# Kernel tuning notes

Hardware: AMD Instinct MI355X
Metric: run time of the kernel (lower is better)

The kernel has to match this reference:

```python
import jax, jax.numpy as jnp
import numpy as np

B, S, H, F, E, TOPK = 4, 2048, 1024, 3584, 8, 2
W_SCALE = 0.02  # keep router logits / activations numerically sane


def setup_inputs() -> dict:
    key = jax.random.key(0)
    k1, k2, k3, k4, k5 = jax.random.split(key, 5)
    return {
        "hidden_states": jax.random.normal(k1, (B, S, H), dtype=jnp.float32),
        "gate_w": jax.random.normal(k2, (E, H), dtype=jnp.float32) * W_SCALE,
        "w1": jax.random.normal(k3, (E, F, H), dtype=jnp.float32) * W_SCALE,
        "w2": jax.random.normal(k4, (E, H, F), dtype=jnp.float32) * W_SCALE,
        "w3": jax.random.normal(k5, (E, F, H), dtype=jnp.float32) * W_SCALE,
        "top_k": TOPK,
    }


def reference(hidden_states, gate_w, w1, w2, w3, top_k):
    b, s, h = hidden_states.shape
    x = hidden_states.reshape(-1, h)                       # [T, H]
    router_logits = x @ gate_w.T                           # [T, E]
    probs = jax.nn.softmax(router_logits.astype(jnp.float32), axis=-1)
    routing_weights, selected_experts = jax.lax.top_k(probs, top_k)  # [T, k]
    routing_weights = routing_weights / routing_weights.sum(axis=-1, keepdims=True)
    routing_weights = routing_weights.astype(x.dtype)
    n_experts = gate_w.shape[0]
    # combine weights: [T, E], zero for unselected experts
    combine = (jax.nn.one_hot(selected_experts, n_experts, dtype=routing_weights.dtype)
               * routing_weights[..., None]).sum(axis=1)
    out = jnp.zeros_like(x)
    for e in range(n_experts):
        hgate = jax.nn.silu(x @ w1[e].T) * (x @ w3[e].T)   # [T, F]
        out = out + (hgate @ w2[e].T) * combine[:, e:e + 1]
    return out.reshape(b, s, h), router_logits
```

## Files before the change

### kernel.cpp

```cpp
#include <hip/hip_runtime.h>
#include <hip/hip_bf16.h>
#include <stdint.h>

#define T_TOK 8192
#define H_DIM 1024
#define F_DIM 3584
#define E_NUM 8

#define BM 128
#define BN 128
#define BK 32
#define LDT 40

typedef __attribute__((ext_vector_type(8))) short bf16x8;
typedef __attribute__((ext_vector_type(4))) float f32x4;

__device__ __forceinline__ short f2bf(float f) {
    union { float f; uint32_t u; } v; v.f = f;
    uint32_t r = v.u + 0x7fffu + ((v.u >> 16) & 1u);
    return (short)(r >> 16);
}

__device__ __forceinline__ void cvt16_store(const float* __restrict__ src, short* dst) {
    const f32x4* p = (const f32x4*)src;
    f32x4 v0 = p[0], v1 = p[1], v2 = p[2], v3 = p[3];
    bf16x8 s0, s1;
    s0[0]=f2bf(v0[0]); s0[1]=f2bf(v0[1]); s0[2]=f2bf(v0[2]); s0[3]=f2bf(v0[3]);
    s0[4]=f2bf(v1[0]); s0[5]=f2bf(v1[1]); s0[6]=f2bf(v1[2]); s0[7]=f2bf(v1[3]);
    s1[0]=f2bf(v2[0]); s1[1]=f2bf(v2[1]); s1[2]=f2bf(v2[2]); s1[3]=f2bf(v2[3]);
    s1[4]=f2bf(v3[0]); s1[5]=f2bf(v3[1]); s1[6]=f2bf(v3[2]); s1[7]=f2bf(v3[3]);
    *(bf16x8*)dst = s0;
    *((bf16x8*)dst + 1) = s1;
}

__device__ __forceinline__ void zero16_store(short* dst) {
    bf16x8 z;
    #pragma unroll
    for (int i = 0; i < 8; i++) z[i] = 0;
    *(bf16x8*)dst = z;
    *((bf16x8*)dst + 1) = z;
}

__global__ void router_kernel(const float* __restrict__ x,
                              const float* __restrict__ gate_w,
                              float* __restrict__ logits_out,
                              int* __restrict__ counts,
                              int* __restrict__ lists,
                              float* __restrict__ wgt) {
    int wave = (blockIdx.x * blockDim.x + threadIdx.x) >> 6;
    int lane = threadIdx.x & 63;
    if (wave >= T_TOK) return;
    const float* xr = x + (size_t)wave * H_DIM;

    float acc[E_NUM];
    #pragma unroll
    for (int e = 0; e < E_NUM; e++) acc[e] = 0.f;

    for (int i = lane; i < H_DIM; i += 64) {
        float xv = xr[i];
        #pragma unroll
        for (int e = 0; e < E_NUM; e++) acc[e] += xv * gate_w[e * H_DIM + i];
    }
    #pragma unroll
    for (int off = 32; off > 0; off >>= 1) {
        #pragma unroll
        for (int e = 0; e < E_NUM; e++) acc[e] += __shfl_xor(acc[e], off);
    }

    if (lane == 0) {
        int t = wave;
        #pragma unroll
        for (int e = 0; e < E_NUM; e++) logits_out[t * E_NUM + e] = acc[e];
        int i0 = 0; float v0 = acc[0];
        #pragma unroll
        for (int e = 1; e < E_NUM; e++) if (acc[e] > v0) { v0 = acc[e]; i0 = e; }
        int i1 = -1; float v1 = -1e30f;
        #pragma unroll
        for (int e = 0; e < E_NUM; e++) if (e != i0 && acc[e] > v1) { v1 = acc[e]; i1 = e; }
        float e1 = __expf(v1 - v0);
        float inv = 1.f / (1.f + e1);
        int a0 = 2 * t, a1 = 2 * t + 1;
        wgt[a0] = inv;
        wgt[a1] = e1 * inv;
        int p0 = atomicAdd(&counts[i0], 1);
        lists[i0 * T_TOK + p0] = a0;
        int p1 = atomicAdd(&counts[i1], 1);
        lists[i1 * T_TOK + p1] = a1;
    }
}

__global__ __launch_bounds__(256, 2)
void gemm1_kernel(const float* __restrict__ x,
                  const float* __restrict__ w1,
                  const float* __restrict__ w3,
                  const int* __restrict__ counts,
                  const int* __restrict__ lists,
                  unsigned short* __restrict__ hgate) {
    const int e = blockIdx.z;
    const int count = counts[e];
    const int mbase = blockIdx.y * BM;
    if (mbase >= count) return;
    const int nbase = blockIdx.x * BN;

    __shared__ short As[BM * LDT];
    __shared__ short B1s[BN * LDT];
    __shared__ short B3s[BN * LDT];

    const int tid = threadIdx.x;
    const int r = tid >> 1;
    const int half = tid & 1;

    const float* arow = nullptr;
    {
        int m = mbase + r;
        if (m < count) {
            int a = lists[e * T_TOK + m];
            arow = x + (size_t)(a >> 1) * H_DIM;
        }
    }
    const float* b1row = w1 + ((size_t)e * F_DIM + (nbase + r)) * H_DIM;
    const float* b3row = w3 + ((size_t)e * F_DIM + (nbase + r)) * H_DIM;

    const int lane = tid & 63;
    const int wid = tid >> 6;
    const int wm = wid >> 1, wn = wid & 1;
    const int lr = lane & 15, lq = lane >> 4;

    f32x4 acc1[4][4], acc3[4][4];
    #pragma unroll
    for (int i = 0; i < 4; i++)
        #pragma unroll
        for (int j = 0; j < 4; j++) {
            acc1[i][j] = (f32x4){0.f, 0.f, 0.f, 0.f};
            acc3[i][j] = (f32x4){0.f, 0.f, 0.f, 0.f};
        }

    for (int k0 = 0; k0 < H_DIM; k0 += BK) {
        const int koff = k0 + half * 16;
        short* adst = &As[r * LDT + half * 16];
        if (arow) cvt16_store(arow + koff, adst); else zero16_store(adst);
        cvt16_store(b1row + koff, &B1s[r * LDT + half * 16]);
        cvt16_store(b3row + koff, &B3s[r * LDT + half * 16]);
        __syncthreads();

        bf16x8 af[4], b1f[4], b3f[4];
        #pragma unroll
        for (int i = 0; i < 4; i++)
            af[i] = *(const bf16x8*)&As[(wm * 64 + i * 16 + lr) * LDT + lq * 8];
        #pragma unroll
        for (int j = 0; j < 4; j++) {
            b1f[j] = *(const bf16x8*)&B1s[(wn * 64 + j * 16 + lr) * LDT + lq * 8];
            b3f[j] = *(const bf16x8*)&B3s[(wn * 64 + j * 16 + lr) * LDT + lq * 8];
        }
        #pragma unroll
        for (int i = 0; i < 4; i++)
            #pragma unroll
            for (int j = 0; j < 4; j++) {
                acc1[i][j] = __builtin_amdgcn_mfma_f32_16x16x32_bf16(af[i], b1f[j], acc1[i][j], 0, 0, 0);
                acc3[i][j] = __builtin_amdgcn_mfma_f32_16x16x32_bf16(af[i], b3f[j], acc3[i][j], 0, 0, 0);
            }
        __syncthreads();
    }

    #pragma unroll
    for (int i = 0; i < 4; i++) {
        #pragma unroll
        for (int rg = 0; rg < 4; rg++) {
            int mm = mbase + wm * 64 + i * 16 + lq * 4 + rg;
            if (mm >= count) continue;
            int a = lists[e * T_TOK + mm];
            unsigned short* hrow = hgate + (size_t)a * F_DIM + nbase;
            #pragma unroll
            for (int j = 0; j < 4; j++) {
                float g = acc1[i][j][rg];
                float u = acc3[i][j][rg];
                float s = (g / (1.f + __expf(-g))) * u;
                hrow[wn * 64 + j * 16 + lr] = (unsigned short)f2bf(s);
            }
        }
    }
}

__global__ __launch_bounds__(256, 2)
void gemm2_kernel(const unsigned short* __restrict__ hgate,
                  const float* __restrict__ w2,
                  const int* __restrict__ counts,
                  const int* __restrict__ lists,
                  const float* __restrict__ wgt,
                  float* __restrict__ out) {
    const int e = blockIdx.z;
    const int count = counts[e];
    const int mbase = blockIdx.y * BM;
    if (mbase >= count) return;
    const int nbase = blockIdx.x * BN;

    __shared__ short As[BM * LDT];
    __shared__ short Bs[BN * LDT];

    const int tid = threadIdx.x;
    const int r = tid >> 1;
    const int half = tid & 1;

    const unsigned short* arow = nullptr;
    {
        int m = mbase + r;
        if (m < count) {
            int a = lists[e * T_TOK + m];
            arow = hgate + (size_t)a * F_DIM;
        }
    }
    const float* brow = w2 + ((size_t)e * H_DIM + (nbase + r)) * F_DIM;

    const int lane = tid & 63;
    const int wid = tid >> 6;
    const int wm = wid >> 1, wn = wid & 1;
    const int lr = lane & 15, lq = lane >> 4;

    f32x4 acc[4][4];
    #pragma unroll
    for (int i = 0; i < 4; i++)
        #pragma unroll
        for (int j = 0; j < 4; j++) acc[i][j] = (f32x4){0.f, 0.f, 0.f, 0.f};

    for (int k0 = 0; k0 < F_DIM; k0 += BK) {
        const int koff = k0 + half * 16;
        short* adst = &As[r * LDT + half * 16];
        if (arow) {
            const bf16x8* p = (const bf16x8*)(arow + koff);
            *(bf16x8*)adst = p[0];
            *((bf16x8*)adst + 1) = p[1];
        } else {
            zero16_store(adst);
        }
        cvt16_store(brow + koff, &Bs[r * LDT + half * 16]);
        __syncthreads();

        bf16x8 af[4], bf[4];
        #pragma unroll
        for (int i = 0; i < 4; i++)
            af[i] = *(const bf16x8*)&As[(wm * 64 + i * 16 + lr) * LDT + lq * 8];
        #pragma unroll
        for (int j = 0; j < 4; j++)
            bf[j] = *(const bf16x8*)&Bs[(wn * 64 + j * 16 + lr) * LDT + lq * 8];
        #pragma unroll
        for (int i = 0; i < 4; i++)
            #pragma unroll
            for (int j = 0; j < 4; j++)
                acc[i][j] = __builtin_amdgcn_mfma_f32_16x16x32_bf16(af[i], bf[j], acc[i][j], 0, 0, 0);
        __syncthreads();
    }

    #pragma unroll
    for (int i = 0; i < 4; i++) {
        #pragma unroll
        for (int rg = 0; rg < 4; rg++) {
            int mm = mbase + wm * 64 + i * 16 + lq * 4 + rg;
            if (mm >= count) continue;
            int a = lists[e * T_TOK + mm];
            float w = wgt[a];
            int t = a >> 1;
            float* orow = out + (size_t)t * H_DIM + nbase;
            #pragma unroll
            for (int j = 0; j < 4; j++)
                atomicAdd(&orow[wn * 64 + j * 16 + lr], acc[i][j][rg] * w);
        }
    }
}

extern "C" void kernel_launch(void* const* d_in, const int* in_sizes, int n_in,
                              void* d_out, int out_size, void* d_ws, size_t ws_size,
                              hipStream_t stream) {
    const float* x      = (const float*)d_in[0];
    const float* gate_w = (const float*)d_in[1];
    const float* w1     = (const float*)d_in[2];
    const float* w2     = (const float*)d_in[3];
    const float* w3     = (const float*)d_in[4];

    float* out    = (float*)d_out;
    float* logits = out + (size_t)T_TOK * H_DIM;

    char* ws = (char*)d_ws;
    int*   counts = (int*)(ws + 0);
    int*   lists  = (int*)(ws + 1024);
    float* wgt    = (float*)(ws + 1024 + (size_t)E_NUM * T_TOK * 4);
    unsigned short* hgate =
        (unsigned short*)(ws + 1024 + (size_t)E_NUM * T_TOK * 4 + (size_t)T_TOK * 2 * 4);

    hipMemsetAsync(counts, 0, E_NUM * sizeof(int), stream);
    hipMemsetAsync(out, 0, (size_t)T_TOK * H_DIM * sizeof(float), stream);

    router_kernel<<<T_TOK / 4, 256, 0, stream>>>(x, gate_w, logits, counts, lists, wgt);

    gemm1_kernel<<<dim3(F_DIM / BN, T_TOK / BM, E_NUM), 256, 0, stream>>>(
        x, w1, w3, counts, lists, hgate);

    gemm2_kernel<<<dim3(H_DIM / BN, T_TOK / BM, E_NUM), 256, 0, stream>>>(
        hgate, w2, counts, lists, wgt, out);
}
```

Measured before the change: 1.360 ms.

## Register-prefetch next K tile and use perm-based bf16 packing in expert GEMMs

Both expert GEMM loops now load the next K-slice of A and B from global memory into registers right after the barrier, so those loads overlap the MFMA work on the current LDS tile instead of stalling at the top of each iteration. The fp32-to-bf16 conversion also switches from round-to-nearest-even to add-0x8000 rounding with a single byte-permute per pair, which cuts ALU instructions but changes tie rounding slightly. The prefetch buffers raise register pressure, which may lower occupancy.

```diff
diff --git a/kernel.cpp b/kernel.cpp
--- a/kernel.cpp
+++ b/kernel.cpp
@@ -21,16 +21,23 @@
     return (short)(r >> 16);
 }
 
-__device__ __forceinline__ void cvt16_store(const float* __restrict__ src, short* dst) {
-    const f32x4* p = (const f32x4*)src;
-    f32x4 v0 = p[0], v1 = p[1], v2 = p[2], v3 = p[3];
-    bf16x8 s0, s1;
-    s0[0]=f2bf(v0[0]); s0[1]=f2bf(v0[1]); s0[2]=f2bf(v0[2]); s0[3]=f2bf(v0[3]);
-    s0[4]=f2bf(v1[0]); s0[5]=f2bf(v1[1]); s0[6]=f2bf(v1[2]); s0[7]=f2bf(v1[3]);
-    s1[0]=f2bf(v2[0]); s1[1]=f2bf(v2[1]); s1[2]=f2bf(v2[2]); s1[3]=f2bf(v2[3]);
-    s1[4]=f2bf(v3[0]); s1[5]=f2bf(v3[1]); s1[6]=f2bf(v3[2]); s1[7]=f2bf(v3[3]);
-    *(bf16x8*)dst = s0;
-    *((bf16x8*)dst + 1) = s1;
+__device__ __forceinline__ uint32_t pack_bf16x2(float a, float b) {
+    union { float f; uint32_t u; } ua, ub;
+    ua.f = a; ub.f = b;
+    return __builtin_amdgcn_perm(ub.u + 0x8000u, ua.u + 0x8000u, 0x07060302u);
+}
+
+__device__ __forceinline__ void cvt_store16(const f32x4* v, short* dst) {
+    uint32_t w[8];
+    #pragma unroll
+    for (int i = 0; i < 4; i++) {
+        w[2*i]   = pack_bf16x2(v[i][0], v[i][1]);
+        w[2*i+1] = pack_bf16x2(v[i][2], v[i][3]);
+    }
+    ((uint32_t*)dst)[0] = w[0]; ((uint32_t*)dst)[1] = w[1];
+    ((uint32_t*)dst)[2] = w[2]; ((uint32_t*)dst)[3] = w[3];
+    ((uint32_t*)dst)[4] = w[4]; ((uint32_t*)dst)[5] = w[5];
+    ((uint32_t*)dst)[6] = w[6]; ((uint32_t*)dst)[7] = w[7];
 }
 
 __device__ __forceinline__ void zero16_store(short* dst) {
@@ -39,6 +46,12 @@
     for (int i = 0; i < 8; i++) z[i] = 0;
     *(bf16x8*)dst = z;
     *((bf16x8*)dst + 1) = z;
+}
+
+__device__ __forceinline__ void load16(f32x4* dst, const float* __restrict__ src) {
+    const f32x4* p = (const f32x4*)src;
+    #pragma unroll
+    for (int i = 0; i < 4; i++) dst[i] = p[i];
 }
 
 __global__ void router_kernel(const float* __restrict__ x,
@@ -135,13 +148,31 @@
             acc3[i][j] = (f32x4){0.f, 0.f, 0.f, 0.f};
         }
 
+    f32x4 ap[4], b1p[4], b3p[4];
+    {
+        const int koff = half * 16;
+        if (arow) load16(ap, arow + koff);
+        load16(b1p, b1row + koff);
+        load16(b3p, b3row + koff);
+    }
+
+    short* adst  = &As[r * LDT + half * 16];
+    short* b1dst = &B1s[r * LDT + half * 16];
+    short* b3dst = &B3s[r * LDT + half * 16];
+
     for (int k0 = 0; k0 < H_DIM; k0 += BK) {
-        const int koff = k0 + half * 16;
-        short* adst = &As[r * LDT + half * 16];
-        if (arow) cvt16_store(arow + koff, adst); else zero16_store(adst);
-        cvt16_store(b1row + koff, &B1s[r * LDT + half * 16]);
-        cvt16_store(b3row + koff, &B3s[r * LDT + half * 16]);
+        if (arow) cvt_store16(ap, adst); else zero16_store(adst);
+        cvt_store16(b1p, b1dst);
+        cvt_store16(b3p, b3dst);
         __syncthreads();
+
+        int kn = k0 + BK;
+        if (kn < H_DIM) {
+            const int koff = kn + half * 16;
+            if (arow) load16(ap, arow + koff);
+            load16(b1p, b1row + koff);
+            load16(b3p, b3row + koff);
+        }
 
         bf16x8 af[4], b1f[4], b3f[4];
         #pragma unroll
@@ -222,18 +253,39 @@
         #pragma unroll
         for (int j = 0; j < 4; j++) acc[i][j] = (f32x4){0.f, 0.f, 0.f, 0.f};
 
-    for (int k0 = 0; k0 < F_DIM; k0 += BK) {
-        const int koff = k0 + half * 16;
-        short* adst = &As[r * LDT + half * 16];
+    bf16x8 a2p[2];
+    f32x4 bp[4];
+    {
+        const int koff = half * 16;
         if (arow) {
             const bf16x8* p = (const bf16x8*)(arow + koff);
-            *(bf16x8*)adst = p[0];
-            *((bf16x8*)adst + 1) = p[1];
+            a2p[0] = p[0]; a2p[1] = p[1];
+        }
+        load16(bp, brow + koff);
+    }
+
+    short* adst = &As[r * LDT + half * 16];
+    short* bdst = &Bs[r * LDT + half * 16];
+
+    for (int k0 = 0; k0 < F_DIM; k0 += BK) {
+        if (arow) {
+            *(bf16x8*)adst = a2p[0];
+            *((bf16x8*)adst + 1) = a2p[1];
         } else {
             zero16_store(adst);
         }
-        cvt16_store(brow + koff, &Bs[r * LDT + half * 16]);
+        cvt_store16(bp, bdst);
         __syncthreads();
+
+        int kn = k0 + BK;
+        if (kn < F_DIM) {
+            const int koff = kn + half * 16;
+            if (arow) {
+                const bf16x8* p = (const bf16x8*)(arow + koff);
+                a2p[0] = p[0]; a2p[1] = p[1];
+            }
+            load16(bp, brow + koff);
+        }
 
         bf16x8 af[4], bf[4];
         #pragma unroll
```

Measured after the change: 1.227 ms. -9.8%, faster.
